# Optimization experiments

Measured on AMD Instinct MI355X. Metric: run time of the kernel, lower is better.

Reference implementation:

```python
import jax, jax.numpy as jnp
import numpy as np

IN_FEATURES = 512
OUT_FEATURES = 512
BATCH = 1024


def setup_inputs() -> dict:
    key = jax.random.key(0)
    k_x, k_bw, k_ww, k_sc, k_tr, k_b = jax.random.split(key, 6)
    std = 1.0 / np.sqrt(IN_FEATURES)
    x = jax.random.normal(k_x, (BATCH, IN_FEATURES), dtype=jnp.float32)
    base_weight = jax.random.uniform(k_bw, (OUT_FEATURES, IN_FEATURES), jnp.float32, -std, std)
    wavelet_weights = jax.random.uniform(k_ww, (OUT_FEATURES, IN_FEATURES), jnp.float32, -std, std)
    # scale initialized to ones in the module; perturb slightly (kept positive) for a non-degenerate test
    scale = jnp.exp(0.1 * jax.random.normal(k_sc, (OUT_FEATURES, IN_FEATURES), dtype=jnp.float32))
    translation = 0.1 * jax.random.normal(k_tr, (OUT_FEATURES, IN_FEATURES), dtype=jnp.float32)
    bias = jax.random.uniform(k_b, (OUT_FEATURES,), jnp.float32, -std, std)
    return {"x": x, "base_weight": base_weight, "wavelet_weights": wavelet_weights,
            "scale": scale, "translation": translation, "bias": bias}


def reference(x, base_weight, wavelet_weights, scale, translation, bias):
    # base branch: SiLU then linear
    base_out = jnp.einsum("bi,oi->bo", jax.nn.silu(x), base_weight)
    # wavelet branch: broadcast x to (batch, out, in)
    xs = (x[:, None, :] - translation[None, :, :]) / scale[None, :, :]  # (B, O, I)
    wavelet = (xs * xs - 1.0) * jnp.exp(-0.5 * xs * xs)  # mexican hat
    wavelet_out = jnp.einsum("boi,oi->bo", wavelet, wavelet_weights)
    return base_out + wavelet_out + bias
```

## Files before the change

kernel.cpp:

```cpp
#include <hip/hip_runtime.h>


constexpr int IN_F  = 512;
constexpr int OUT_F = 512;
constexpr int BATCH = 1024;
constexpr int BT = 64, OT = 64;
constexpr int KS = 4;
constexpr int KR = IN_F / KS;
constexpr int IT = 16;
constexpr int PITCH = IT + 4;
constexpr int NCH = KR / IT;
constexpr int BO  = BATCH * OUT_F;

#define LOG2E 1.44269504088897f
#define C2f   (-0.72134752044448f)
#define NC2f  ( 0.72134752044448f)
#define RQf   (-0.84083003f)

typedef float v2f __attribute__((ext_vector_type(2)));

__device__ __forceinline__ float fexp2(float v) { return __builtin_amdgcn_exp2f(v); }
__device__ __forceinline__ float frcp(float v)  { return __builtin_amdgcn_rcpf(v); }
__device__ __forceinline__ v2f pkfma(v2f a, v2f b, v2f c) {
#if __has_builtin(__builtin_elementwise_fma)
  return __builtin_elementwise_fma(a, b, c);
#else
  v2f r; r.x = fmaf(a.x, b.x, c.x); r.y = fmaf(a.y, b.y, c.y); return r;
#endif
}
__device__ __forceinline__ float fsilu(float v) {
  return v * frcp(1.f + fexp2(v * -LOG2E));
}

__global__ __launch_bounds__(256, 4)
void wkan_main(const float* __restrict__ x, const float* __restrict__ basew,
               const float* __restrict__ wavew, const float* __restrict__ scale,
               const float* __restrict__ transl, const float* __restrict__ bias,
               float* __restrict__ partial, float* __restrict__ out, int use_ws)
{
  __shared__ float lx [BT * PITCH];
  __shared__ float lsx[BT * PITCH];
  __shared__ float la [OT * PITCH];
  __shared__ float lm [OT * PITCH];
  __shared__ float ln [OT * PITCH];
  __shared__ float lq [OT * PITCH];
  __shared__ float lb [OT * PITCH];

  const int tid = threadIdx.x;
  const int b0 = blockIdx.x * BT;
  const int o0 = blockIdx.y * OT;
  const int ks = blockIdx.z;
  const int k0 = ks * KR;

  const int srow = tid >> 2;
  const int sc4  = (tid & 3) * 4;
  const int lofs = srow * PITCH + sc4;

  const int to = tid & 15;
  const int tb = tid >> 4;

  v2f zz; zz.x = 0.f; zz.y = 0.f;
  v2f acc[4][4];
#pragma unroll
  for (int r = 0; r < 4; ++r)
#pragma unroll
    for (int c = 0; c < 4; ++c) acc[r][c] = zz;

  for (int kc = 0; kc < NCH; ++kc) {
    const int g = k0 + kc * IT + sc4;
    __syncthreads();
    {
      float4 xv = *(const float4*)(x + (size_t)(b0 + srow) * IN_F + g);
      float4 sx;
      sx.x = fsilu(xv.x); sx.y = fsilu(xv.y); sx.z = fsilu(xv.z); sx.w = fsilu(xv.w);
      *(float4*)(lx  + lofs) = xv;
      *(float4*)(lsx + lofs) = sx;

      float4 sv = *(const float4*)(scale  + (size_t)(o0 + srow) * IN_F + g);
      float4 tv = *(const float4*)(transl + (size_t)(o0 + srow) * IN_F + g);
      float4 av, mv, nv;
      {
        float a2, a2t;
        a2 = C2f * frcp(sv.x * sv.x); a2t = a2 * tv.x;
        av.x = a2; mv.x = -2.f * a2t; nv.x = fmaf(a2t, tv.x, NC2f);
        a2 = C2f * frcp(sv.y * sv.y); a2t = a2 * tv.y;
        av.y = a2; mv.y = -2.f * a2t; nv.y = fmaf(a2t, tv.y, NC2f);
        a2 = C2f * frcp(sv.z * sv.z); a2t = a2 * tv.z;
        av.z = a2; mv.z = -2.f * a2t; nv.z = fmaf(a2t, tv.z, NC2f);
        a2 = C2f * frcp(sv.w * sv.w); a2t = a2 * tv.w;
        av.w = a2; mv.w = -2.f * a2t; nv.w = fmaf(a2t, tv.w, NC2f);
      }
      *(float4*)(la + lofs) = av;
      *(float4*)(lm + lofs) = mv;
      *(float4*)(ln + lofs) = nv;

      float4 wv = *(const float4*)(wavew + (size_t)(o0 + srow) * IN_F + g);
      float4 qv;
      qv.x = wv.x * RQf; qv.y = wv.y * RQf; qv.z = wv.z * RQf; qv.w = wv.w * RQf;
      *(float4*)(lq + lofs) = qv;

      float4 bv = *(const float4*)(basew + (size_t)(o0 + srow) * IN_F + g);
      *(float4*)(lb + lofs) = bv;
    }
    __syncthreads();

    for (int ii = 0; ii < IT; ii += 4) {
      float4 xr[4], sr[4], x2[4];
#pragma unroll
      for (int r = 0; r < 4; ++r) {
        const int row = (tb + 16 * r) * PITCH + ii;
        xr[r] = *(const float4*)(lx + row);
        sr[r] = *(const float4*)(lsx + row);
        x2[r].x = xr[r].x * xr[r].x;
        x2[r].y = xr[r].y * xr[r].y;
        x2[r].z = xr[r].z * xr[r].z;
        x2[r].w = xr[r].w * xr[r].w;
      }
#pragma unroll
      for (int c = 0; c < 4; ++c) {
        const int orow = (to + 16 * c) * PITCH + ii;
        float4 A = *(const float4*)(la + orow);
        float4 M = *(const float4*)(lm + orow);
        float4 N = *(const float4*)(ln + orow);
        float4 Q = *(const float4*)(lq + orow);
        float4 B = *(const float4*)(lb + orow);
        v2f Al = {A.x, A.y}, Ah = {A.z, A.w};
        v2f Ml = {M.x, M.y}, Mh = {M.z, M.w};
        v2f Nl = {N.x, N.y}, Nh = {N.z, N.w};
        v2f Ql = {Q.x, Q.y}, Qh = {Q.z, Q.w};
        v2f Bl = {B.x, B.y}, Bh = {B.z, B.w};
#pragma unroll
        for (int r = 0; r < 4; ++r) {
          v2f xl  = {xr[r].x, xr[r].y}, xh  = {xr[r].z, xr[r].w};
          v2f x2l = {x2[r].x, x2[r].y}, x2h = {x2[r].z, x2[r].w};
          v2f sl  = {sr[r].x, sr[r].y}, sh  = {sr[r].z, sr[r].w};
          v2f p, e, gg;
          p = pkfma(Al, x2l, pkfma(Ml, xl, Nl));
          e.x = fexp2(p.x); e.y = fexp2(p.y);
          gg = p * Ql;
          acc[r][c] = pkfma(gg, e, acc[r][c]);
          acc[r][c] = pkfma(sl, Bl, acc[r][c]);
          p = pkfma(Ah, x2h, pkfma(Mh, xh, Nh));
          e.x = fexp2(p.x); e.y = fexp2(p.y);
          gg = p * Qh;
          acc[r][c] = pkfma(gg, e, acc[r][c]);
          acc[r][c] = pkfma(sh, Bh, acc[r][c]);
        }
      }
    }
  }

#pragma unroll
  for (int r = 0; r < 4; ++r) {
    const int br = b0 + tb + 16 * r;
#pragma unroll
    for (int c = 0; c < 4; ++c) {
      const int oc = o0 + to + 16 * c;
      float res = acc[r][c].x + acc[r][c].y;
      if (use_ws) {
        partial[(size_t)ks * BO + (size_t)br * OUT_F + oc] = res;
      } else {
        if (ks == 0) res += bias[oc];
        atomicAdd(out + (size_t)br * OUT_F + oc, res);
      }
    }
  }
}

__global__ __launch_bounds__(256)
void wkan_reduce(const float* __restrict__ partial, const float* __restrict__ bias,
                 float* __restrict__ out)
{
  const int i4 = (blockIdx.x * 256 + threadIdx.x) * 4;
  float4 a = *(const float4*)(partial + i4);
  float4 b = *(const float4*)(partial + (size_t)BO + i4);
  float4 c = *(const float4*)(partial + (size_t)2 * BO + i4);
  float4 d = *(const float4*)(partial + (size_t)3 * BO + i4);
  float4 bi = *(const float4*)(bias + (i4 & (OUT_F - 1)));
  float4 r;
  r.x = a.x + b.x + c.x + d.x + bi.x;
  r.y = a.y + b.y + c.y + d.y + bi.y;
  r.z = a.z + b.z + c.z + d.z + bi.z;
  r.w = a.w + b.w + c.w + d.w + bi.w;
  *(float4*)(out + i4) = r;
}

extern "C" void kernel_launch(void* const* d_in, const int* in_sizes, int n_in,
                              void* d_out, int out_size, void* d_ws, size_t ws_size,
                              hipStream_t stream) {
  const float* x  = (const float*)d_in[0];
  const float* bw = (const float*)d_in[1];
  const float* ww = (const float*)d_in[2];
  const float* sc = (const float*)d_in[3];
  const float* tr = (const float*)d_in[4];
  const float* bi = (const float*)d_in[5];
  float* out = (float*)d_out;

  const int use_ws = ws_size >= (size_t)KS * BO * sizeof(float) ? 1 : 0;
  if (!use_ws) {
    hipMemsetAsync(d_out, 0, (size_t)out_size * sizeof(float), stream);
  }
  dim3 grid(BATCH / BT, OUT_F / OT, KS);
  wkan_main<<<grid, dim3(256), 0, stream>>>(x, bw, ww, sc, tr, bi,
                                            (float*)d_ws, out, use_ws);
  if (use_ws) {
    wkan_reduce<<<dim3(BO / 1024), dim3(256), 0, stream>>>((const float*)d_ws, bi, out);
  }
}
```

Baseline: 117.6 us.

## Replace hardware exp2 with packed polynomial exp2 and double K-split

Moves the wavelet exponent out of the transcendental unit. It now computes exp2 with a magic-number round plus a degree-4 packed polynomial and bit-shift exponent assembly, all on packed-FMA ALU ops. The quadratic exponent is now formed from translation directly as a*(x-t)^2+c, which drops two LDS arrays. The K split is doubled to 8, so there are more blocks, and the reduce kernel sums 8 partials. In exchange the kernel does more VALU work per element, the polynomial has lower accuracy for very negative exponents, and the workspace traffic is larger.

After: 143.3 us. 1.22x slower.

```diff
diff --git a/kernel.cpp b/kernel.cpp
--- a/kernel.cpp
+++ b/kernel.cpp
@@ -5,7 +5,7 @@
 constexpr int OUT_F = 512;
 constexpr int BATCH = 1024;
 constexpr int BT = 64, OT = 64;
-constexpr int KS = 4;
+constexpr int KS = 8;
 constexpr int KR = IN_F / KS;
 constexpr int IT = 16;
 constexpr int PITCH = IT + 4;
@@ -16,17 +16,14 @@
 #define C2f   (-0.72134752044448f)
 #define NC2f  ( 0.72134752044448f)
 #define RQf   (-0.84083003f)
+#define MAGICf 12582912.0f
 
 typedef float v2f __attribute__((ext_vector_type(2)));
 
 __device__ __forceinline__ float fexp2(float v) { return __builtin_amdgcn_exp2f(v); }
 __device__ __forceinline__ float frcp(float v)  { return __builtin_amdgcn_rcpf(v); }
 __device__ __forceinline__ v2f pkfma(v2f a, v2f b, v2f c) {
-#if __has_builtin(__builtin_elementwise_fma)
   return __builtin_elementwise_fma(a, b, c);
-#else
-  v2f r; r.x = fmaf(a.x, b.x, c.x); r.y = fmaf(a.y, b.y, c.y); return r;
-#endif
 }
 __device__ __forceinline__ float fsilu(float v) {
   return v * frcp(1.f + fexp2(v * -LOG2E));
@@ -41,8 +38,7 @@
   __shared__ float lx [BT * PITCH];
   __shared__ float lsx[BT * PITCH];
   __shared__ float la [OT * PITCH];
-  __shared__ float lm [OT * PITCH];
-  __shared__ float ln [OT * PITCH];
+  __shared__ float lt [OT * PITCH];
   __shared__ float lq [OT * PITCH];
   __shared__ float lb [OT * PITCH];
 
@@ -59,12 +55,19 @@
   const int to = tid & 15;
   const int tb = tid >> 4;
 
-  v2f zz; zz.x = 0.f; zz.y = 0.f;
+  const v2f NC2v  = {NC2f, NC2f};
+  const v2f MAGv  = {MAGICf, MAGICf};
+  const v2f P4 = {0.0096181291f, 0.0096181291f};
+  const v2f P3 = {0.0555041087f, 0.0555041087f};
+  const v2f P2 = {0.2402265070f, 0.2402265070f};
+  const v2f P1 = {0.6931471806f, 0.6931471806f};
+  const v2f P0 = {1.0f, 1.0f};
+
   v2f acc[4][4];
 #pragma unroll
   for (int r = 0; r < 4; ++r)
 #pragma unroll
-    for (int c = 0; c < 4; ++c) acc[r][c] = zz;
+    for (int c = 0; c < 4; ++c) acc[r][c] = (v2f){0.f, 0.f};
 
   for (int kc = 0; kc < NCH; ++kc) {
     const int g = k0 + kc * IT + sc4;
@@ -77,22 +80,15 @@
       *(float4*)(lsx + lofs) = sx;
 
       float4 sv = *(const float4*)(scale  + (size_t)(o0 + srow) * IN_F + g);
+      float4 av;
+      av.x = C2f * frcp(sv.x * sv.x);
+      av.y = C2f * frcp(sv.y * sv.y);
+      av.z = C2f * frcp(sv.z * sv.z);
+      av.w = C2f * frcp(sv.w * sv.w);
+      *(float4*)(la + lofs) = av;
+
       float4 tv = *(const float4*)(transl + (size_t)(o0 + srow) * IN_F + g);
-      float4 av, mv, nv;
-      {
-        float a2, a2t;
-        a2 = C2f * frcp(sv.x * sv.x); a2t = a2 * tv.x;
-        av.x = a2; mv.x = -2.f * a2t; nv.x = fmaf(a2t, tv.x, NC2f);
-        a2 = C2f * frcp(sv.y * sv.y); a2t = a2 * tv.y;
-        av.y = a2; mv.y = -2.f * a2t; nv.y = fmaf(a2t, tv.y, NC2f);
-        a2 = C2f * frcp(sv.z * sv.z); a2t = a2 * tv.z;
-        av.z = a2; mv.z = -2.f * a2t; nv.z = fmaf(a2t, tv.z, NC2f);
-        a2 = C2f * frcp(sv.w * sv.w); a2t = a2 * tv.w;
-        av.w = a2; mv.w = -2.f * a2t; nv.w = fmaf(a2t, tv.w, NC2f);
-      }
-      *(float4*)(la + lofs) = av;
-      *(float4*)(lm + lofs) = mv;
-      *(float4*)(ln + lofs) = nv;
+      *(float4*)(lt + lofs) = tv;
 
       float4 wv = *(const float4*)(wavew + (size_t)(o0 + srow) * IN_F + g);
       float4 qv;
@@ -105,46 +101,48 @@
     __syncthreads();
 
     for (int ii = 0; ii < IT; ii += 4) {
-      float4 xr[4], sr[4], x2[4];
+      float4 xr[4], sr[4];
 #pragma unroll
       for (int r = 0; r < 4; ++r) {
         const int row = (tb + 16 * r) * PITCH + ii;
         xr[r] = *(const float4*)(lx + row);
         sr[r] = *(const float4*)(lsx + row);
-        x2[r].x = xr[r].x * xr[r].x;
-        x2[r].y = xr[r].y * xr[r].y;
-        x2[r].z = xr[r].z * xr[r].z;
-        x2[r].w = xr[r].w * xr[r].w;
       }
 #pragma unroll
       for (int c = 0; c < 4; ++c) {
         const int orow = (to + 16 * c) * PITCH + ii;
         float4 A = *(const float4*)(la + orow);
-        float4 M = *(const float4*)(lm + orow);
-        float4 N = *(const float4*)(ln + orow);
+        float4 T = *(const float4*)(lt + orow);
         float4 Q = *(const float4*)(lq + orow);
         float4 B = *(const float4*)(lb + orow);
         v2f Al = {A.x, A.y}, Ah = {A.z, A.w};
-        v2f Ml = {M.x, M.y}, Mh = {M.z, M.w};
-        v2f Nl = {N.x, N.y}, Nh = {N.z, N.w};
+        v2f Tl = {T.x, T.y}, Th = {T.z, T.w};
         v2f Ql = {Q.x, Q.y}, Qh = {Q.z, Q.w};
         v2f Bl = {B.x, B.y}, Bh = {B.z, B.w};
 #pragma unroll
         for (int r = 0; r < 4; ++r) {
-          v2f xl  = {xr[r].x, xr[r].y}, xh  = {xr[r].z, xr[r].w};
-          v2f x2l = {x2[r].x, x2[r].y}, x2h = {x2[r].z, x2[r].w};
-          v2f sl  = {sr[r].x, sr[r].y}, sh  = {sr[r].z, sr[r].w};
-          v2f p, e, gg;
-          p = pkfma(Al, x2l, pkfma(Ml, xl, Nl));
-          e.x = fexp2(p.x); e.y = fexp2(p.y);
-          gg = p * Ql;
-          acc[r][c] = pkfma(gg, e, acc[r][c]);
-          acc[r][c] = pkfma(sl, Bl, acc[r][c]);
-          p = pkfma(Ah, x2h, pkfma(Mh, xh, Nh));
-          e.x = fexp2(p.x); e.y = fexp2(p.y);
-          gg = p * Qh;
-          acc[r][c] = pkfma(gg, e, acc[r][c]);
-          acc[r][c] = pkfma(sh, Bh, acc[r][c]);
+          v2f xl = {xr[r].x, xr[r].y}, xh = {xr[r].z, xr[r].w};
+          v2f sl = {sr[r].x, sr[r].y}, sh = {sr[r].z, sr[r].w};
+#pragma unroll
+          for (int h = 0; h < 2; ++h) {
+            v2f X = h ? xh : xl, S = h ? sh : sl;
+            v2f Aa = h ? Ah : Al, Tt = h ? Th : Tl;
+            v2f Qq = h ? Qh : Ql, Bb = h ? Bh : Bl;
+            v2f d  = X - Tt;
+            v2f ad = Aa * d;
+            v2f p  = pkfma(ad, d, NC2v);
+            v2f tt = p + MAGv;
+            v2f nf = tt - MAGv;
+            v2f f  = p - nf;
+            v2f poly = pkfma(pkfma(pkfma(pkfma(P4, f, P3), f, P2), f, P1), f, P0);
+            unsigned s0 = (__float_as_uint(tt.x) << 23) + 0x3F800000u;
+            unsigned s1 = (__float_as_uint(tt.y) << 23) + 0x3F800000u;
+            v2f sc2 = {__uint_as_float(s0), __uint_as_float(s1)};
+            v2f pq = p * Qq;
+            v2f pe = pq * poly;
+            acc[r][c] = pkfma(pe, sc2, acc[r][c]);
+            acc[r][c] = pkfma(S, Bb, acc[r][c]);
+          }
         }
       }
     }
@@ -172,16 +170,12 @@
                  float* __restrict__ out)
 {
   const int i4 = (blockIdx.x * 256 + threadIdx.x) * 4;
-  float4 a = *(const float4*)(partial + i4);
-  float4 b = *(const float4*)(partial + (size_t)BO + i4);
-  float4 c = *(const float4*)(partial + (size_t)2 * BO + i4);
-  float4 d = *(const float4*)(partial + (size_t)3 * BO + i4);
-  float4 bi = *(const float4*)(bias + (i4 & (OUT_F - 1)));
-  float4 r;
-  r.x = a.x + b.x + c.x + d.x + bi.x;
-  r.y = a.y + b.y + c.y + d.y + bi.y;
-  r.z = a.z + b.z + c.z + d.z + bi.z;
-  r.w = a.w + b.w + c.w + d.w + bi.w;
+  float4 r = *(const float4*)(bias + (i4 & (OUT_F - 1)));
+#pragma unroll
+  for (int k = 0; k < KS; ++k) {
+    float4 a = *(const float4*)(partial + (size_t)k * BO + i4);
+    r.x += a.x; r.y += a.y; r.z += a.z; r.w += a.w;
+  }
   *(float4*)(out + i4) = r;
 }
 
```
